# Performance work log

Hardware: AMD Instinct MI355X
Metric: run time of the kernel (lower is better)

## Reference

```python
import jax, jax.numpy as jnp
import numpy as np
from jax import lax

EPS = 1e-06
NUM_FEATURES = 2048


def _welford(xr, mean0, var0):
    """Sequential Welford running mean/var, exactly matching the torch loop.

    xr: [N, F] rows processed one at a time.
    Update for the n-th observation (n starts at 1):
      if n > 1: var = (n-2)/(n-1)*var + (obs-mean)^2/n
      mean += (obs-mean)/n
    """
    n_rows = xr.shape[0]

    def step(carry, inp):
        mean, var = carry
        obs, n = inp
        nf = n.astype(xr.dtype)
        d = obs - mean
        # safe denominator so the unselected branch at n==1 is finite
        var_new = jnp.where(n > 1, (nf - 2.0) / jnp.maximum(nf - 1.0, 1.0) * var + d * d / nf, var)
        mean_new = mean + d / nf
        return (mean_new, var_new), None

    ns = jnp.arange(1, n_rows + 1, dtype=jnp.int32)
    (mean, var), _ = lax.scan(step, (mean0, var0), (xr, ns))
    return mean, var


def setup_inputs() -> dict:
    key = jax.random.key(0)
    x = jax.random.normal(key, (8192, NUM_FEATURES), dtype=jnp.float32)
    running_mean = jnp.zeros((NUM_FEATURES,), dtype=jnp.float32)
    running_var = jnp.ones((NUM_FEATURES,), dtype=jnp.float32)
    return {"x": x, "running_mean": running_mean, "running_var": running_var}


def reference(x, running_mean, running_var):
    xr = x.reshape(-1, NUM_FEATURES)
    mean, var = _welford(xr, running_mean, running_var)
    # normalize with the FINAL running stats (loop completes before return)
    return (x - mean) / jnp.sqrt(var + EPS)
```

## Files before the change

kernel.cpp:

```cpp
#include <hip/hip_runtime.h>

constexpr int F = 2048;
constexpr int NROWS = 8192;
constexpr float EPS = 1e-6f;
constexpr int STRIDE4 = F / 4;

typedef float nfloat4 __attribute__((ext_vector_type(4)));

__global__ __launch_bounds__(256) void reduce_kernel(const float* __restrict__ x,
                                                     float* __restrict__ acc) {
    __shared__ float4 lS[3 * 64];
    __shared__ float4 lQ[3 * 64];

    const int lc = threadIdx.x & 63;
    const int sg = threadIdx.x >> 6;
    const int c4 = blockIdx.x * 64 + lc;
    const int row0 = blockIdx.y * 64 + sg * 16;
    const float4* __restrict__ xv = reinterpret_cast<const float4*>(x);

    float4 s = make_float4(0.f, 0.f, 0.f, 0.f);
    float4 q = make_float4(0.f, 0.f, 0.f, 0.f);

    size_t base = (size_t)row0 * STRIDE4 + (size_t)c4;
#pragma unroll
    for (int r = 0; r < 16; ++r) {
        float4 v = xv[base + (size_t)r * STRIDE4];
        s.x += v.x;  s.y += v.y;  s.z += v.z;  s.w += v.w;
        q.x = fmaf(v.x, v.x, q.x);
        q.y = fmaf(v.y, v.y, q.y);
        q.z = fmaf(v.z, v.z, q.z);
        q.w = fmaf(v.w, v.w, q.w);
    }

    if (sg != 0) {
        lS[(sg - 1) * 64 + lc] = s;
        lQ[(sg - 1) * 64 + lc] = q;
    }
    __syncthreads();

    if (sg == 0) {
#pragma unroll
        for (int k = 0; k < 3; ++k) {
            float4 t = lS[k * 64 + lc];
            float4 u = lQ[k * 64 + lc];
            s.x += t.x;  s.y += t.y;  s.z += t.z;  s.w += t.w;
            q.x += u.x;  q.y += u.y;  q.z += u.z;  q.w += u.w;
        }
        float* __restrict__ sum   = acc;
        float* __restrict__ sumsq = acc + F;
        const int c = c4 * 4;
        atomicAdd(&sum[c + 0], s.x);
        atomicAdd(&sum[c + 1], s.y);
        atomicAdd(&sum[c + 2], s.z);
        atomicAdd(&sum[c + 3], s.w);
        atomicAdd(&sumsq[c + 0], q.x);
        atomicAdd(&sumsq[c + 1], q.y);
        atomicAdd(&sumsq[c + 2], q.z);
        atomicAdd(&sumsq[c + 3], q.w);
    }
}

__global__ __launch_bounds__(256) void norm_kernel(const float* __restrict__ x,
                                                   const float* __restrict__ acc,
                                                   float* __restrict__ out) {
    const int lc = threadIdx.x & 63;
    const int sg = threadIdx.x >> 6;
    const int c4 = blockIdx.x * 64 + lc;
    const int row0 = blockIdx.y * 64 + sg * 16;
    const float4* __restrict__ xv = reinterpret_cast<const float4*>(x);
    nfloat4* __restrict__ ov      = reinterpret_cast<nfloat4*>(out);

    const float4 S1 = reinterpret_cast<const float4*>(acc)[c4];
    const float4 S2 = reinterpret_cast<const float4*>(acc + F)[c4];

    const float invN  = 1.0f / (float)NROWS;
    const float invN1 = 1.0f / (float)(NROWS - 1);

    float4 r4, b4;
    {
        const float mx = S1.x * invN;
        const float my = S1.y * invN;
        const float mz = S1.z * invN;
        const float mw = S1.w * invN;
        const float vx = fmaxf((S2.x - S1.x * mx) * invN1, 0.0f);
        const float vy = fmaxf((S2.y - S1.y * my) * invN1, 0.0f);
        const float vz = fmaxf((S2.z - S1.z * mz) * invN1, 0.0f);
        const float vw = fmaxf((S2.w - S1.w * mw) * invN1, 0.0f);
        r4.x = rsqrtf(vx + EPS);
        r4.y = rsqrtf(vy + EPS);
        r4.z = rsqrtf(vz + EPS);
        r4.w = rsqrtf(vw + EPS);
        b4.x = -mx * r4.x;
        b4.y = -my * r4.y;
        b4.z = -mz * r4.z;
        b4.w = -mw * r4.w;
    }

    const size_t base = (size_t)row0 * STRIDE4 + (size_t)c4;
#pragma unroll
    for (int r = 0; r < 16; ++r) {
        const size_t idx = base + (size_t)r * STRIDE4;
        const float4 t = xv[idx];
        nfloat4 o;
        o.x = fmaf(t.x, r4.x, b4.x);
        o.y = fmaf(t.y, r4.y, b4.y);
        o.z = fmaf(t.z, r4.z, b4.z);
        o.w = fmaf(t.w, r4.w, b4.w);
        __builtin_nontemporal_store(o, &ov[idx]);
    }
}

extern "C" void kernel_launch(void* const* d_in, const int* in_sizes, int n_in,
                              void* d_out, int out_size, void* d_ws, size_t ws_size,
                              hipStream_t stream) {
    const float* x = (const float*)d_in[0];
    float* out = (float*)d_out;
    float* acc = (float*)d_ws;

    (void)hipMemsetAsync(d_ws, 0, 2 * F * sizeof(float), stream);

    reduce_kernel<<<dim3(8, NROWS / 64), 256, 0, stream>>>(x, acc);
    norm_kernel<<<dim3(8, NROWS / 64), 256, 0, stream>>>(x, acc, out);
}
```

Baseline: 130.6 us.

## Fuse reduce and normalize into one kernel with a grid barrier and register-held tile

Merges the statistics reduction and the normalization into a single kernel. Each thread keeps its 16 loaded float4 values in registers, and all blocks meet at a global atomic-counter spin barrier. After the barrier they read the final sums, compute scale and bias, and write the output without reading x from memory a second time. This removes one full pass over x and one kernel launch, and loads now use nontemporal hints. In exchange it depends on all 1024 blocks being resident at once (launch bounds request 4 blocks per CU), uses more registers per thread, and adds spin-wait latency at the barrier.

```diff
diff --git a/kernel.cpp b/kernel.cpp
--- a/kernel.cpp
+++ b/kernel.cpp
@@ -4,11 +4,14 @@
 constexpr int NROWS = 8192;
 constexpr float EPS = 1e-6f;
 constexpr int STRIDE4 = F / 4;
+constexpr unsigned NBLOCKS = 8u * (NROWS / 64);
 
 typedef float nfloat4 __attribute__((ext_vector_type(4)));
 
-__global__ __launch_bounds__(256) void reduce_kernel(const float* __restrict__ x,
-                                                     float* __restrict__ acc) {
+__global__ __launch_bounds__(256, 4) void fused_kernel(const float* __restrict__ x,
+                                                       float* __restrict__ acc,
+                                                       unsigned* __restrict__ ctr,
+                                                       float* __restrict__ out) {
     __shared__ float4 lS[3 * 64];
     __shared__ float4 lQ[3 * 64];
 
@@ -16,20 +19,23 @@
     const int sg = threadIdx.x >> 6;
     const int c4 = blockIdx.x * 64 + lc;
     const int row0 = blockIdx.y * 64 + sg * 16;
-    const float4* __restrict__ xv = reinterpret_cast<const float4*>(x);
 
+    const nfloat4* __restrict__ xv = reinterpret_cast<const nfloat4*>(x);
+    const size_t base = (size_t)row0 * STRIDE4 + (size_t)c4;
+
+    nfloat4 v[16];
     float4 s = make_float4(0.f, 0.f, 0.f, 0.f);
     float4 q = make_float4(0.f, 0.f, 0.f, 0.f);
 
-    size_t base = (size_t)row0 * STRIDE4 + (size_t)c4;
 #pragma unroll
     for (int r = 0; r < 16; ++r) {
-        float4 v = xv[base + (size_t)r * STRIDE4];
-        s.x += v.x;  s.y += v.y;  s.z += v.z;  s.w += v.w;
-        q.x = fmaf(v.x, v.x, q.x);
-        q.y = fmaf(v.y, v.y, q.y);
-        q.z = fmaf(v.z, v.z, q.z);
-        q.w = fmaf(v.w, v.w, q.w);
+        const nfloat4 t = __builtin_nontemporal_load(&xv[base + (size_t)r * STRIDE4]);
+        v[r] = t;
+        s.x += t.x;  s.y += t.y;  s.z += t.z;  s.w += t.w;
+        q.x = fmaf(t.x, t.x, q.x);
+        q.y = fmaf(t.y, t.y, q.y);
+        q.z = fmaf(t.z, t.z, q.z);
+        q.w = fmaf(t.w, t.w, q.w);
     }
 
     if (sg != 0) {
@@ -41,8 +47,8 @@
     if (sg == 0) {
 #pragma unroll
         for (int k = 0; k < 3; ++k) {
-            float4 t = lS[k * 64 + lc];
-            float4 u = lQ[k * 64 + lc];
+            const float4 t = lS[k * 64 + lc];
+            const float4 u = lQ[k * 64 + lc];
             s.x += t.x;  s.y += t.y;  s.z += t.z;  s.w += t.w;
             q.x += u.x;  q.y += u.y;  q.z += u.z;  q.w += u.w;
         }
@@ -58,55 +64,65 @@
         atomicAdd(&sumsq[c + 2], q.z);
         atomicAdd(&sumsq[c + 3], q.w);
     }
-}
 
-__global__ __launch_bounds__(256) void norm_kernel(const float* __restrict__ x,
-                                                   const float* __restrict__ acc,
-                                                   float* __restrict__ out) {
-    const int lc = threadIdx.x & 63;
-    const int sg = threadIdx.x >> 6;
-    const int c4 = blockIdx.x * 64 + lc;
-    const int row0 = blockIdx.y * 64 + sg * 16;
-    const float4* __restrict__ xv = reinterpret_cast<const float4*>(x);
-    nfloat4* __restrict__ ov      = reinterpret_cast<nfloat4*>(out);
+    __syncthreads();
+    if (threadIdx.x == 0) {
+        __threadfence();
+        atomicAdd(ctr, 1u);
+        for (int it = 0; it < (1 << 22); ++it) {
+            if (__hip_atomic_load(ctr, __ATOMIC_ACQUIRE, __HIP_MEMORY_SCOPE_AGENT) >= NBLOCKS)
+                break;
+            __builtin_amdgcn_s_sleep(32);
+        }
+    }
+    __syncthreads();
 
-    const float4 S1 = reinterpret_cast<const float4*>(acc)[c4];
-    const float4 S2 = reinterpret_cast<const float4*>(acc + F)[c4];
+    if (sg == 0) {
+        const int c = c4 * 4;
+        float S1[4], S2[4];
+#pragma unroll
+        for (int k = 0; k < 4; ++k) {
+            S1[k] = __hip_atomic_load(&acc[c + k],     __ATOMIC_RELAXED, __HIP_MEMORY_SCOPE_AGENT);
+            S2[k] = __hip_atomic_load(&acc[F + c + k], __ATOMIC_RELAXED, __HIP_MEMORY_SCOPE_AGENT);
+        }
+        const float invN  = 1.0f / (float)NROWS;
+        const float invN1 = 1.0f / (float)(NROWS - 1);
+        float4 r4, b4;
+        {
+            const float mx = S1[0] * invN;
+            const float my = S1[1] * invN;
+            const float mz = S1[2] * invN;
+            const float mw = S1[3] * invN;
+            const float vx = fmaxf((S2[0] - S1[0] * mx) * invN1, 0.0f);
+            const float vy = fmaxf((S2[1] - S1[1] * my) * invN1, 0.0f);
+            const float vz = fmaxf((S2[2] - S1[2] * mz) * invN1, 0.0f);
+            const float vw = fmaxf((S2[3] - S1[3] * mw) * invN1, 0.0f);
+            r4.x = rsqrtf(vx + EPS);
+            r4.y = rsqrtf(vy + EPS);
+            r4.z = rsqrtf(vz + EPS);
+            r4.w = rsqrtf(vw + EPS);
+            b4.x = -mx * r4.x;
+            b4.y = -my * r4.y;
+            b4.z = -mz * r4.z;
+            b4.w = -mw * r4.w;
+        }
+        lS[lc] = r4;
+        lQ[lc] = b4;
+    }
+    __syncthreads();
 
-    const float invN  = 1.0f / (float)NROWS;
-    const float invN1 = 1.0f / (float)(NROWS - 1);
-
-    float4 r4, b4;
-    {
-        const float mx = S1.x * invN;
-        const float my = S1.y * invN;
-        const float mz = S1.z * invN;
-        const float mw = S1.w * invN;
-        const float vx = fmaxf((S2.x - S1.x * mx) * invN1, 0.0f);
-        const float vy = fmaxf((S2.y - S1.y * my) * invN1, 0.0f);
-        const float vz = fmaxf((S2.z - S1.z * mz) * invN1, 0.0f);
-        const float vw = fmaxf((S2.w - S1.w * mw) * invN1, 0.0f);
-        r4.x = rsqrtf(vx + EPS);
-        r4.y = rsqrtf(vy + EPS);
-        r4.z = rsqrtf(vz + EPS);
-        r4.w = rsqrtf(vw + EPS);
-        b4.x = -mx * r4.x;
-        b4.y = -my * r4.y;
-        b4.z = -mz * r4.z;
-        b4.w = -mw * r4.w;
-    }
-
-    const size_t base = (size_t)row0 * STRIDE4 + (size_t)c4;
+    const float4 r4 = lS[lc];
+    const float4 b4 = lQ[lc];
+    nfloat4* __restrict__ ov = reinterpret_cast<nfloat4*>(out);
 #pragma unroll
     for (int r = 0; r < 16; ++r) {
-        const size_t idx = base + (size_t)r * STRIDE4;
-        const float4 t = xv[idx];
+        const nfloat4 t = v[r];
         nfloat4 o;
         o.x = fmaf(t.x, r4.x, b4.x);
         o.y = fmaf(t.y, r4.y, b4.y);
         o.z = fmaf(t.z, r4.z, b4.z);
         o.w = fmaf(t.w, r4.w, b4.w);
-        __builtin_nontemporal_store(o, &ov[idx]);
+        __builtin_nontemporal_store(o, &ov[base + (size_t)r * STRIDE4]);
     }
 }
 
@@ -114,11 +130,11 @@
                               void* d_out, int out_size, void* d_ws, size_t ws_size,
                               hipStream_t stream) {
     const float* x = (const float*)d_in[0];
-    float* out = (float*)d_out;
-    float* acc = (float*)d_ws;
+    float* out    = (float*)d_out;
+    float* acc    = (float*)d_ws;
+    unsigned* ctr = (unsigned*)(acc + 2 * F);
 
-    (void)hipMemsetAsync(d_ws, 0, 2 * F * sizeof(float), stream);
+    (void)hipMemsetAsync(d_ws, 0, (2 * F + 4) * sizeof(float), stream);
 
-    reduce_kernel<<<dim3(8, NROWS / 64), 256, 0, stream>>>(x, acc);
-    norm_kernel<<<dim3(8, NROWS / 64), 256, 0, stream>>>(x, acc, out);
+    fused_kernel<<<dim3(8, NROWS / 64), 256, 0, stream>>>(x, acc, ctr, out);
 }
```

Result: slower. 246.4 us (+88.7%).
